# Performance work log

Measured on AMD Instinct MI355X. Metric: run time of the kernel, lower is better.

The kernel has to match this reference:

```python
import jax, jax.numpy as jnp
import numpy as np

BN_EPS = 1e-5


def setup_inputs() -> dict:
    key = jax.random.key(0)
    ks = jax.random.split(key, 6)
    b, c_out, c_high = 8, 256, 512
    h1 = w1 = 64
    h2 = w2 = 32
    return {
        "fms_low": jax.random.normal(ks[0], (b, c_out, h1, w1), jnp.float32),
        "fms_high": jax.random.normal(ks[1], (b, c_high, h2, w2), jnp.float32),
        "w_conv": jax.random.normal(ks[2], (c_out, c_high), jnp.float32) * (1.0 / np.sqrt(c_high)),
        "bn_gamma": jnp.ones((c_out,), jnp.float32),
        "bn_beta": jnp.zeros((c_out,), jnp.float32),
        "bn_mean": jnp.zeros((c_out,), jnp.float32),
        "bn_var": jnp.ones((c_out,), jnp.float32),
        "fc1_w": jax.random.normal(ks[3], (c_out // 4, c_out), jnp.float32) * (1.0 / np.sqrt(c_out)),
        "fc1_b": jnp.zeros((c_out // 4,), jnp.float32),
        "fc2_w": jax.random.normal(ks[4], (c_out // 4, c_out), jnp.float32) * (1.0 / np.sqrt(c_out)),
        "fc2_b": jnp.zeros((c_out // 4,), jnp.float32),
        "scale": jax.random.normal(ks[5], (1,), jnp.float32),
    }


def reference(fms_low, fms_high, w_conv, bn_gamma, bn_beta, bn_mean, bn_var,
              fc1_w, fc1_b, fc2_w, fc2_b, scale):
    b, c, h1, w1 = fms_low.shape
    # conv_high: 1x1 conv (no bias) + BN (inference) + ReLU
    x = jnp.einsum('bchw,oc->bohw', fms_high, w_conv)  # [b, 256, h2, w2]
    inv = bn_gamma / jnp.sqrt(bn_var + BN_EPS)
    x = x * inv[None, :, None, None] + (bn_beta - bn_mean * inv)[None, :, None, None]
    x = jax.nn.relu(x)
    # raw row-major reshapes, matching torch .view(b, -1, C)
    feat_low = fms_low.reshape(b, -1, c)    # [b, N_low, 256]
    feat_high = x.reshape(b, -1, c)         # [b, N_high, 256]
    mid_low = feat_low @ fc1_w.T + fc1_b    # [b, N_low, 64]
    mid_high = feat_high @ fc2_w.T + fc2_b  # [b, N_high, 64]
    energy = jnp.einsum('bnd,bmd->bnm', mid_low, mid_high)  # [b, N_low, N_high]
    attn = jax.nn.softmax(energy, axis=-1)
    # bmm(feat_high^T, attn^T) -> [b, 256, N_low]
    mid = jnp.einsum('bmc,bnm->bcn', feat_high, attn).reshape(b, c, h1, w1)
    return scale[0] * mid
```

## Files before the change

kernel.cpp:

```cpp
#include <hip/hip_runtime.h>
#include <hip/hip_bf16.h>

typedef __bf16 v8bf __attribute__((ext_vector_type(8)));
typedef float  v4f  __attribute__((ext_vector_type(4)));

typedef __attribute__((address_space(3))) void       lds_vd;
typedef __attribute__((address_space(1))) const void gbl_vd;

#define MFMA16(a, b, c) __builtin_amdgcn_mfma_f32_16x16x32_bf16(a, b, c, 0, 0, 0)

__device__ __forceinline__ void split_hl(float v, __bf16* h, __bf16* l) {
    __bf16 hh = (__bf16)v;
    *h = hh;
    *l = (__bf16)(v - (float)hh);
}

__device__ __forceinline__ int swz_idx(int row, int col) {
    return row * 64 + ((((col >> 3) ^ (row & 7))) << 3) + (col & 7);
}
__device__ __forceinline__ const __bf16* frag_ptr(const __bf16* base, int row, int g) {
    return base + row * 64 + ((g ^ (row & 7)) << 3);
}


__global__ __launch_bounds__(256) void k_conv(
    const float* __restrict__ FH, const float* __restrict__ W,
    const float* __restrict__ gamma, const float* __restrict__ beta,
    const float* __restrict__ mean, const float* __restrict__ var,
    __bf16* __restrict__ Xhi, __bf16* __restrict__ Xlo, __bf16* __restrict__ VT)
{
    __shared__ __align__(16) __bf16 Ah[64 * 64];
    __shared__ __align__(16) __bf16 Al[64 * 64];
    __shared__ __align__(16) __bf16 Bh[64 * 64];
    __shared__ __align__(16) __bf16 Bl[64 * 64];
    __shared__ float invl[64], shl[64];

    const int tid = threadIdx.x, lane = tid & 63, w = tid >> 6;
    const int l15 = lane & 15, quad = lane >> 4;
    const int u0 = blockIdx.x * 16, o0 = blockIdx.y * 64, b = blockIdx.z;
    const float* FHb = FH + (size_t)b * 524288;

    if (tid < 64) {
        const int o = o0 + tid;
        const float iv = gamma[o] * rsqrtf(var[o] + 1e-5f);
        invl[tid] = iv;
        shl[tid] = beta[o] - mean[o] * iv;
    }

    const int ao = tid >> 2, aseg = tid & 3;
    float wreg[16], freg[16];
    {
        const float* wp = W + (size_t)(o0 + ao) * 512 + aseg * 16;
        #pragma unroll
        for (int q = 0; q < 4; ++q) {
            float4 f = ((const float4*)wp)[q];
            wreg[4*q] = f.x; wreg[4*q+1] = f.y; wreg[4*q+2] = f.z; wreg[4*q+3] = f.w;
        }
        const float* fp = FHb + (size_t)lane * 1024 + w * 256 + u0;
        #pragma unroll
        for (int q = 0; q < 4; ++q) {
            float4 f = ((const float4*)fp)[q];
            freg[4*q] = f.x; freg[4*q+1] = f.y; freg[4*q+2] = f.z; freg[4*q+3] = f.w;
        }
    }

    v4f acc[2][2];
    #pragma unroll
    for (int i = 0; i < 2; ++i)
        #pragma unroll
        for (int j = 0; j < 2; ++j) { v4f z = {0.f,0.f,0.f,0.f}; acc[i][j] = z; }
    const int oh = w >> 1, nh = w & 1;

    for (int ch = 0; ch < 8; ++ch) {
        if (ch) __syncthreads();
        #pragma unroll
        for (int z = 0; z < 2; ++z) {
            v8bf hv, lv;
            #pragma unroll
            for (int e = 0; e < 8; ++e) {
                __bf16 h, l; split_hl(wreg[8*z + e], &h, &l);
                hv[e] = h; lv[e] = l;
            }
            const int gi = (2*aseg + z) ^ (ao & 7);
            *(v8bf*)(Ah + ao*64 + (gi << 3)) = hv;
            *(v8bf*)(Al + ao*64 + (gi << 3)) = lv;
        }
        #pragma unroll
        for (int ul = 0; ul < 16; ++ul) {
            __bf16 h, l; split_hl(freg[ul], &h, &l);
            const int idx = (w*16 + ul)*64 + (((lane >> 3) ^ (ul & 7)) << 3) + (lane & 7);
            Bh[idx] = h; Bl[idx] = l;
        }
        __syncthreads();
        if (ch < 7) {
            const int c1 = (ch + 1) * 64;
            const float* wp = W + (size_t)(o0 + ao) * 512 + c1 + aseg * 16;
            #pragma unroll
            for (int q = 0; q < 4; ++q) {
                float4 f = ((const float4*)wp)[q];
                wreg[4*q] = f.x; wreg[4*q+1] = f.y; wreg[4*q+2] = f.z; wreg[4*q+3] = f.w;
            }
            const float* fp = FHb + (size_t)(c1 + lane) * 1024 + w * 256 + u0;
            #pragma unroll
            for (int q = 0; q < 4; ++q) {
                float4 f = ((const float4*)fp)[q];
                freg[4*q] = f.x; freg[4*q+1] = f.y; freg[4*q+2] = f.z; freg[4*q+3] = f.w;
            }
        }
        #pragma unroll
        for (int ks = 0; ks < 2; ++ks) {
            const int g = 4*ks + quad;
            v8bf a_h[2], a_l[2], b_h[2], b_l[2];
            #pragma unroll
            for (int i = 0; i < 2; ++i) {
                const int row = oh*32 + i*16 + l15;
                a_h[i] = *(const v8bf*)frag_ptr(Ah, row, g);
                a_l[i] = *(const v8bf*)frag_ptr(Al, row, g);
            }
            #pragma unroll
            for (int j = 0; j < 2; ++j) {
                const int row = nh*32 + j*16 + l15;
                b_h[j] = *(const v8bf*)frag_ptr(Bh, row, g);
                b_l[j] = *(const v8bf*)frag_ptr(Bl, row, g);
            }
            #pragma unroll
            for (int i = 0; i < 2; ++i)
                #pragma unroll
                for (int j = 0; j < 2; ++j) {
                    acc[i][j] = MFMA16(a_h[i], b_h[j], acc[i][j]);
                    acc[i][j] = MFMA16(a_h[i], b_l[j], acc[i][j]);
                    acc[i][j] = MFMA16(a_l[i], b_h[j], acc[i][j]);
                }
        }
    }
    __syncthreads();

    #pragma unroll
    for (int i = 0; i < 2; ++i)
        #pragma unroll
        for (int j = 0; j < 2; ++j)
            #pragma unroll
            for (int r = 0; r < 4; ++r) {
                const int row = oh*32 + i*16 + quad*4 + r;
                const int col = nh*32 + j*16 + l15;
                float v = acc[i][j][r] * invl[row] + shl[row];
                v = fmaxf(v, 0.f);
                __bf16 h, l; split_hl(v, &h, &l);
                const int idx = swz_idx(row, col);
                Ah[idx] = h; Al[idx] = l;
            }
    __syncthreads();
    {
        const int o = tid >> 2, pv = tid & 3;
        const size_t gbase = ((size_t)b*256 + o0 + o) * 1024 + pv*256 + u0;
        #pragma unroll
        for (int z = 0; z < 2; ++z) {
            const int gi = (2*pv + z) ^ (o & 7);
            v8bf h = *(v8bf*)(Ah + o*64 + (gi << 3));
            v8bf l = *(v8bf*)(Al + o*64 + (gi << 3));
            *(v8bf*)(Xhi + gbase + z*8) = h;
            *(v8bf*)(Xlo + gbase + z*8) = l;
        }
    }
    {
        const int ul = tid >> 4, s = tid & 15;
        __bf16 tmp[16];
        #pragma unroll
        for (int k = 0; k < 16; ++k) {
            const int m = s*16 + k;
            const int row = m >> 2;
            const int col = (m & 3)*16 + ul;
            tmp[k] = Ah[swz_idx(row, col)];
        }
        __bf16* vp = VT + ((size_t)b*256 + u0 + ul) * 1024 + 4*o0 + s*16;
        *(v8bf*)(vp)     = *(v8bf*)(tmp);
        *(v8bf*)(vp + 8) = *(v8bf*)(tmp + 8);
    }
}

__global__ __launch_bounds__(256) void k_proj32(
    const float* __restrict__ Feat, const float* __restrict__ Wfc,
    const float* __restrict__ bfc,
    __bf16* __restrict__ Ohi, __bf16* __restrict__ Olo)
{
    __shared__ __align__(16) __bf16 Ah[128 * 64], Al[128 * 64];
    __shared__ __align__(16) __bf16 Bh[64 * 64],  Bl[64 * 64];
    const int tid = threadIdx.x, lane = tid & 63, w = tid >> 6;
    const int l15 = lane & 15, quad = lane >> 4;
    const int r0 = blockIdx.x * 128;
    const int arow = tid >> 1, ahalf = tid & 1;
    const int brow = tid >> 2, bseg = tid & 3;

    float areg[32], breg[16];
    {
        const float* ap = Feat + (size_t)(r0 + arow) * 256 + ahalf * 32;
        #pragma unroll
        for (int q = 0; q < 8; ++q) {
            float4 f = ((const float4*)ap)[q];
            areg[4*q] = f.x; areg[4*q+1] = f.y; areg[4*q+2] = f.z; areg[4*q+3] = f.w;
        }
        const float* bp = Wfc + (size_t)brow * 256 + bseg * 16;
        #pragma unroll
        for (int q = 0; q < 4; ++q) {
            float4 f = ((const float4*)bp)[q];
            breg[4*q] = f.x; breg[4*q+1] = f.y; breg[4*q+2] = f.z; breg[4*q+3] = f.w;
        }
    }
    v4f acc[2][4];
    #pragma unroll
    for (int i = 0; i < 2; ++i)
        #pragma unroll
        for (int j = 0; j < 4; ++j) { v4f z = {0.f,0.f,0.f,0.f}; acc[i][j] = z; }

    for (int ch = 0; ch < 4; ++ch) {
        if (ch) __syncthreads();
        #pragma unroll
        for (int z = 0; z < 4; ++z) {
            v8bf hv, lv;
            #pragma unroll
            for (int e = 0; e < 8; ++e) {
                __bf16 h, l; split_hl(areg[8*z + e], &h, &l);
                hv[e] = h; lv[e] = l;
            }
            const int gi = (4*ahalf + z) ^ (arow & 7);
            *(v8bf*)(Ah + arow*64 + (gi << 3)) = hv;
            *(v8bf*)(Al + arow*64 + (gi << 3)) = lv;
        }
        #pragma unroll
        for (int z = 0; z < 2; ++z) {
            v8bf hv, lv;
            #pragma unroll
            for (int e = 0; e < 8; ++e) {
                __bf16 h, l; split_hl(breg[8*z + e], &h, &l);
                hv[e] = h; lv[e] = l;
            }
            const int gi = (2*bseg + z) ^ (brow & 7);
            *(v8bf*)(Bh + brow*64 + (gi << 3)) = hv;
            *(v8bf*)(Bl + brow*64 + (gi << 3)) = lv;
        }
        __syncthreads();
        if (ch < 3) {
            const int c1 = (ch + 1) * 64;
            const float* ap = Feat + (size_t)(r0 + arow) * 256 + c1 + ahalf * 32;
            #pragma unroll
            for (int q = 0; q < 8; ++q) {
                float4 f = ((const float4*)ap)[q];
                areg[4*q] = f.x; areg[4*q+1] = f.y; areg[4*q+2] = f.z; areg[4*q+3] = f.w;
            }
            const float* bp = Wfc + (size_t)brow * 256 + c1 + bseg * 16;
            #pragma unroll
            for (int q = 0; q < 4; ++q) {
                float4 f = ((const float4*)bp)[q];
                breg[4*q] = f.x; breg[4*q+1] = f.y; breg[4*q+2] = f.z; breg[4*q+3] = f.w;
            }
        }
        #pragma unroll
        for (int ks = 0; ks < 2; ++ks) {
            const int g = 4*ks + quad;
            v8bf a_h[2], a_l[2], b_h[4], b_l[4];
            #pragma unroll
            for (int i = 0; i < 2; ++i) {
                const int row = w*32 + i*16 + l15;
                a_h[i] = *(const v8bf*)frag_ptr(Ah, row, g);
                a_l[i] = *(const v8bf*)frag_ptr(Al, row, g);
            }
            #pragma unroll
            for (int j = 0; j < 4; ++j) {
                const int row = j*16 + l15;
                b_h[j] = *(const v8bf*)frag_ptr(Bh, row, g);
                b_l[j] = *(const v8bf*)frag_ptr(Bl, row, g);
            }
            #pragma unroll
            for (int i = 0; i < 2; ++i)
                #pragma unroll
                for (int j = 0; j < 4; ++j) {
                    acc[i][j] = MFMA16(a_h[i], b_h[j], acc[i][j]);
                    acc[i][j] = MFMA16(a_h[i], b_l[j], acc[i][j]);
                    acc[i][j] = MFMA16(a_l[i], b_h[j], acc[i][j]);
                }
        }
    }
    __syncthreads();
    #pragma unroll
    for (int j = 0; j < 4; ++j) {
        const float bias = bfc[j*16 + l15];
        #pragma unroll
        for (int i = 0; i < 2; ++i)
            #pragma unroll
            for (int r = 0; r < 4; ++r) {
                const int row = w*32 + i*16 + quad*4 + r;
                const int col = j*16 + l15;
                __bf16 h, l; split_hl(acc[i][j][r] + bias, &h, &l);
                const int idx = swz_idx(row, col);
                Ah[idx] = h; Al[idx] = l;
            }
    }
    __syncthreads();
    {
        const int row = tid >> 1, half = tid & 1;
        __bf16* oh_ = Ohi + (size_t)(r0 + row) * 64 + half * 32;
        __bf16* ol_ = Olo + (size_t)(r0 + row) * 64 + half * 32;
        #pragma unroll
        for (int z = 0; z < 4; ++z) {
            const int gi = (4*half + z) ^ (row & 7);
            *(v8bf*)(oh_ + z*8) = *(v8bf*)(Ah + row*64 + (gi << 3));
            *(v8bf*)(ol_ + z*8) = *(v8bf*)(Al + row*64 + (gi << 3));
        }
    }
}

__global__ __launch_bounds__(256) void k_projbf(
    const __bf16* __restrict__ Fhi, const __bf16* __restrict__ Flo,
    const float* __restrict__ Wfc, const float* __restrict__ bfc,
    __bf16* __restrict__ Ohi, __bf16* __restrict__ Olo)
{
    __shared__ __align__(16) __bf16 Ah[32 * 64], Al[32 * 64];
    __shared__ __align__(16) __bf16 Bh[64 * 64], Bl[64 * 64];
    const int tid = threadIdx.x, lane = tid & 63, w = tid >> 6;
    const int l15 = lane & 15, quad = lane >> 4;
    const int r0 = blockIdx.x * 32;
    const int srow = tid >> 3, sg = tid & 7;
    const int brow = tid >> 2, bseg = tid & 3;

    float breg[16];
    v8bf ha, la;
    {
        ha = *(const v8bf*)(Fhi + (size_t)(r0 + srow) * 256 + sg * 8);
        la = *(const v8bf*)(Flo + (size_t)(r0 + srow) * 256 + sg * 8);
        const float* bp = Wfc + (size_t)brow * 256 + bseg * 16;
        #pragma unroll
        for (int q = 0; q < 4; ++q) {
            float4 f = ((const float4*)bp)[q];
            breg[4*q] = f.x; breg[4*q+1] = f.y; breg[4*q+2] = f.z; breg[4*q+3] = f.w;
        }
    }
    v4f acc[2];
    { v4f z = {0.f,0.f,0.f,0.f}; acc[0] = z; acc[1] = z; }
    const int mt = w >> 1, nh = w & 1;

    for (int ch = 0; ch < 4; ++ch) {
        if (ch) __syncthreads();
        {
            const int gi = sg ^ (srow & 7);
            *(v8bf*)(Ah + srow*64 + (gi << 3)) = ha;
            *(v8bf*)(Al + srow*64 + (gi << 3)) = la;
        }
        #pragma unroll
        for (int z = 0; z < 2; ++z) {
            v8bf hv, lv;
            #pragma unroll
            for (int e = 0; e < 8; ++e) {
                __bf16 h, l; split_hl(breg[8*z + e], &h, &l);
                hv[e] = h; lv[e] = l;
            }
            const int gi = (2*bseg + z) ^ (brow & 7);
            *(v8bf*)(Bh + brow*64 + (gi << 3)) = hv;
            *(v8bf*)(Bl + brow*64 + (gi << 3)) = lv;
        }
        __syncthreads();
        if (ch < 3) {
            const int c1 = (ch + 1) * 64;
            ha = *(const v8bf*)(Fhi + (size_t)(r0 + srow) * 256 + c1 + sg * 8);
            la = *(const v8bf*)(Flo + (size_t)(r0 + srow) * 256 + c1 + sg * 8);
            const float* bp = Wfc + (size_t)brow * 256 + c1 + bseg * 16;
            #pragma unroll
            for (int q = 0; q < 4; ++q) {
                float4 f = ((const float4*)bp)[q];
                breg[4*q] = f.x; breg[4*q+1] = f.y; breg[4*q+2] = f.z; breg[4*q+3] = f.w;
            }
        }
        #pragma unroll
        for (int ks = 0; ks < 2; ++ks) {
            const int g = 4*ks + quad;
            const int arow = mt*16 + l15;
            v8bf a_h = *(const v8bf*)frag_ptr(Ah, arow, g);
            v8bf a_l = *(const v8bf*)frag_ptr(Al, arow, g);
            #pragma unroll
            for (int j = 0; j < 2; ++j) {
                const int row = (nh*2 + j)*16 + l15;
                v8bf b_h = *(const v8bf*)frag_ptr(Bh, row, g);
                v8bf b_l = *(const v8bf*)frag_ptr(Bl, row, g);
                acc[j] = MFMA16(a_h, b_h, acc[j]);
                acc[j] = MFMA16(a_h, b_l, acc[j]);
                acc[j] = MFMA16(a_l, b_h, acc[j]);
            }
        }
    }
    __syncthreads();
    #pragma unroll
    for (int j = 0; j < 2; ++j) {
        const float bias = bfc[(nh*2 + j)*16 + l15];
        #pragma unroll
        for (int r = 0; r < 4; ++r) {
            const int row = mt*16 + quad*4 + r;
            const int col = (nh*2 + j)*16 + l15;
            __bf16 h, l; split_hl(acc[j][r] + bias, &h, &l);
            const int idx = swz_idx(row, col);
            Ah[idx] = h; Al[idx] = l;
        }
    }
    __syncthreads();
    {
        const int row = tid >> 3, g = tid & 7;
        const int gi = g ^ (row & 7);
        *(v8bf*)(Ohi + (size_t)(r0 + row) * 64 + g*8) = *(v8bf*)(Ah + row*64 + (gi << 3));
        *(v8bf*)(Olo + (size_t)(r0 + row) * 64 + g*8) = *(v8bf*)(Al + row*64 + (gi << 3));
    }
}

__global__ __launch_bounds__(256, 4) void k_attn(
    const __bf16* __restrict__ MLhi, const __bf16* __restrict__ MLlo,
    const __bf16* __restrict__ MHhi, const __bf16* __restrict__ MHlo,
    const __bf16* __restrict__ VT,
    const float* __restrict__ scale_p,
    float* __restrict__ out)
{
    __shared__ __align__(16) __bf16 Khi[32 * 64];
    __shared__ __align__(16) __bf16 Klo[32 * 64];
    __shared__ __align__(16) __bf16 Vs[256 * 32];
    __shared__ __align__(16) __bf16 Ps[4][16 * 32];
    __shared__ float lsh[4][16];

    const int tid = threadIdx.x, lane = tid & 63, w = tid >> 6;
    const int l15 = lane & 15, quad = lane >> 4;
    const int b = blockIdx.x & 7, qtb = blockIdx.x >> 3;
    const int q0 = qtb * 64;

    v8bf qhi[2], qlo[2];
    {
        const __bf16* qp  = MLhi + ((size_t)(b*4096 + q0 + w*16 + l15)) * 64;
        const __bf16* qlp = MLlo + ((size_t)(b*4096 + q0 + w*16 + l15)) * 64;
        #pragma unroll
        for (int h = 0; h < 2; ++h) {
            qhi[h] = *(const v8bf*)(qp + h*32 + quad*8);
            qlo[h] = *(const v8bf*)(qlp + h*32 + quad*8);
        }
    }

    const char* Khg = (const char*)(MHhi + (size_t)b * 65536);
    const char* Klg = (const char*)(MHlo + (size_t)b * 65536);
    const char* Vg  = (const char*)(VT + (size_t)b * 262144);
    const int offK = (lane >> 3) * 128 + (((lane & 7) ^ ((lane >> 3) & 7)) << 4);
    const int offV = (lane >> 2) * 2048 + ((((lane & 3) ^ ((lane >> 3) & 3))) << 4);

    v4f oacc[4][4];
    #pragma unroll
    for (int qt = 0; qt < 4; ++qt)
        #pragma unroll
        for (int cb = 0; cb < 4; ++cb) { v4f z = {0.f,0.f,0.f,0.f}; oacc[qt][cb] = z; }
    float lrow[4] = {0.f, 0.f, 0.f, 0.f};

    for (int ch = 0; ch < 32; ++ch) {
        const int m0 = ch * 32;
        if (ch) __syncthreads();
        if (w < 4) {
            __builtin_amdgcn_global_load_lds((gbl_vd*)(Khg + m0*128 + w*1024 + offK),
                                             (lds_vd*)((char*)Khi + w*1024), 16, 0, 0);
            __builtin_amdgcn_global_load_lds((gbl_vd*)(Klg + m0*128 + w*1024 + offK),
                                             (lds_vd*)((char*)Klo + w*1024), 16, 0, 0);
        }
        #pragma unroll
        for (int i = w; i < 16; i += 4)
            __builtin_amdgcn_global_load_lds((gbl_vd*)(Vg + m0*2 + i*32768 + offV),
                                             (lds_vd*)((char*)Vs + i*1024), 16, 0, 0);
        __syncthreads();

        float S[2][4];
        #pragma unroll
        for (int mb = 0; mb < 2; ++mb) {
            v4f sacc = {0.f, 0.f, 0.f, 0.f};
            #pragma unroll
            for (int h = 0; h < 2; ++h) {
                const int row = mb*16 + l15, g = 4*h + quad;
                v8bf kh = *(const v8bf*)frag_ptr(Khi, row, g);
                v8bf kl = *(const v8bf*)frag_ptr(Klo, row, g);
                sacc = MFMA16(qhi[h], kh, sacc);
                sacc = MFMA16(qhi[h], kl, sacc);
                sacc = MFMA16(qlo[h], kh, sacc);
            }
            #pragma unroll
            for (int r = 0; r < 4; ++r) S[mb][r] = sacc[r];
        }

        #pragma unroll
        for (int mb = 0; mb < 2; ++mb)
            #pragma unroll
            for (int r = 0; r < 4; ++r) {
                const float p = __expf(S[mb][r]);
                S[mb][r] = p;
                lrow[r] += p;
            }
        #pragma unroll
        for (int mb = 0; mb < 2; ++mb)
            #pragma unroll
            for (int r = 0; r < 4; ++r) {
                const int row = quad*4 + r;
                const int slot = (mb*2 + (l15 >> 3)) ^ ((row >> 1) & 3);
                Ps[w][row*32 + (slot << 3) + (l15 & 7)] = (__bf16)S[mb][r];
            }
        __syncthreads();

        v8bf pa[4];
        #pragma unroll
        for (int qt = 0; qt < 4; ++qt)
            pa[qt] = *(const v8bf*)(Ps[qt] + l15*32 + ((quad ^ ((l15 >> 1) & 3)) << 3));
        #pragma unroll
        for (int cb = 0; cb < 4; ++cb) {
            const int vrow = w*64 + cb*16 + l15;
            v8bf vv = *(const v8bf*)(Vs + vrow*32 + ((quad ^ ((vrow >> 1) & 3)) << 3));
            #pragma unroll
            for (int qt = 0; qt < 4; ++qt)
                oacc[qt][cb] = MFMA16(pa[qt], vv, oacc[qt][cb]);
        }
    }

    #pragma unroll
    for (int r = 0; r < 4; ++r) {
        float s = lrow[r];
        #pragma unroll
        for (int d = 1; d < 16; d <<= 1) s += __shfl_xor(s, d, 64);
        lrow[r] = s;
    }
    if (l15 == 0) {
        #pragma unroll
        for (int r = 0; r < 4; ++r) lsh[w][quad*4 + r] = lrow[r];
    }
    __syncthreads();

    const float scl = scale_p[0];
    float inv[4][4];
    #pragma unroll
    for (int qt = 0; qt < 4; ++qt)
        #pragma unroll
        for (int r = 0; r < 4; ++r) inv[qt][r] = scl / lsh[qt][quad*4 + r];
    float* outb = out + (size_t)b * 256 * 4096;
    #pragma unroll
    for (int cb = 0; cb < 4; ++cb) {
        const int c = w*64 + cb*16 + l15;
        #pragma unroll
        for (int qt = 0; qt < 4; ++qt) {
            float4 v;
            v.x = oacc[qt][cb][0] * inv[qt][0];
            v.y = oacc[qt][cb][1] * inv[qt][1];
            v.z = oacc[qt][cb][2] * inv[qt][2];
            v.w = oacc[qt][cb][3] * inv[qt][3];
            *(float4*)(outb + (size_t)c * 4096 + q0 + qt*16 + quad*4) = v;
        }
    }
}

extern "C" void kernel_launch(void* const* d_in, const int* in_sizes, int n_in,
                              void* d_out, int out_size, void* d_ws, size_t ws_size,
                              hipStream_t stream)
{
    const float* fms_low  = (const float*)d_in[0];
    const float* fms_high = (const float*)d_in[1];
    const float* w_conv   = (const float*)d_in[2];
    const float* gamma    = (const float*)d_in[3];
    const float* beta     = (const float*)d_in[4];
    const float* mean     = (const float*)d_in[5];
    const float* var      = (const float*)d_in[6];
    const float* fc1_w    = (const float*)d_in[7];
    const float* fc1_b    = (const float*)d_in[8];
    const float* fc2_w    = (const float*)d_in[9];
    const float* fc2_b    = (const float*)d_in[10];
    const float* scale    = (const float*)d_in[11];
    float* out = (float*)d_out;

    __bf16* Xhi  = (__bf16*)d_ws;
    __bf16* Xlo  = Xhi  + (size_t)8*256*1024;
    __bf16* VT   = Xlo  + (size_t)8*256*1024;
    __bf16* MLhi = VT   + (size_t)8*256*1024;
    __bf16* MLlo = MLhi + (size_t)8*4096*64;
    __bf16* MHhi = MLlo + (size_t)8*4096*64;
    __bf16* MHlo = MHhi + (size_t)8*1024*64;

    k_conv<<<dim3(16, 4, 8), 256, 0, stream>>>(fms_high, w_conv, gamma, beta,
                                               mean, var, Xhi, Xlo, VT);
    k_projbf<<<dim3(256), 256, 0, stream>>>(Xhi, Xlo, fc2_w, fc2_b, MHhi, MHlo);
    k_proj32<<<dim3(256), 256, 0, stream>>>(fms_low, fc1_w, fc1_b, MLhi, MLlo);
    k_attn<<<dim3(512), 256, 0, stream>>>(MLhi, MLlo, MHhi, MHlo, VT, scale, out);
}
```

Measured before the change: 195.7 us.

## Double-buffer conv and attention tiles, restructure projections and attention P layout

The conv kernel now double-buffers its LDS tiles, which drops one barrier per chunk. Both projection kernels now hold the whole split weight in LDS and stream A fragments straight from global memory with no chunk loop. The attention kernel prefetches the next K/V chunk into a second LDS buffer, computes S transposed, and moves P through lane shuffles instead of shared memory. It also makes each wave own 16 queries across all 256 channels, which removes the cross-wave row-sum reduction. The cost is more LDS per block, lower occupancy, and output stores that are scalar and strided.

```diff
diff --git a/kernel.cpp b/kernel.cpp
--- a/kernel.cpp
+++ b/kernel.cpp
@@ -29,10 +29,10 @@
     const float* __restrict__ mean, const float* __restrict__ var,
     __bf16* __restrict__ Xhi, __bf16* __restrict__ Xlo, __bf16* __restrict__ VT)
 {
-    __shared__ __align__(16) __bf16 Ah[64 * 64];
-    __shared__ __align__(16) __bf16 Al[64 * 64];
-    __shared__ __align__(16) __bf16 Bh[64 * 64];
-    __shared__ __align__(16) __bf16 Bl[64 * 64];
+    __shared__ __align__(16) __bf16 Ah[2][64 * 64];
+    __shared__ __align__(16) __bf16 Al[2][64 * 64];
+    __shared__ __align__(16) __bf16 Bh[2][64 * 64];
+    __shared__ __align__(16) __bf16 Bl[2][64 * 64];
     __shared__ float invl[64], shl[64];
 
     const int tid = threadIdx.x, lane = tid & 63, w = tid >> 6;
@@ -72,7 +72,7 @@
     const int oh = w >> 1, nh = w & 1;
 
     for (int ch = 0; ch < 8; ++ch) {
-        if (ch) __syncthreads();
+        const int bf = ch & 1;
         #pragma unroll
         for (int z = 0; z < 2; ++z) {
             v8bf hv, lv;
@@ -82,14 +82,14 @@
                 hv[e] = h; lv[e] = l;
             }
             const int gi = (2*aseg + z) ^ (ao & 7);
-            *(v8bf*)(Ah + ao*64 + (gi << 3)) = hv;
-            *(v8bf*)(Al + ao*64 + (gi << 3)) = lv;
+            *(v8bf*)(Ah[bf] + ao*64 + (gi << 3)) = hv;
+            *(v8bf*)(Al[bf] + ao*64 + (gi << 3)) = lv;
         }
         #pragma unroll
         for (int ul = 0; ul < 16; ++ul) {
             __bf16 h, l; split_hl(freg[ul], &h, &l);
             const int idx = (w*16 + ul)*64 + (((lane >> 3) ^ (ul & 7)) << 3) + (lane & 7);
-            Bh[idx] = h; Bl[idx] = l;
+            Bh[bf][idx] = h; Bl[bf][idx] = l;
         }
         __syncthreads();
         if (ch < 7) {
@@ -114,14 +114,14 @@
             #pragma unroll
             for (int i = 0; i < 2; ++i) {
                 const int row = oh*32 + i*16 + l15;
-                a_h[i] = *(const v8bf*)frag_ptr(Ah, row, g);
-                a_l[i] = *(const v8bf*)frag_ptr(Al, row, g);
+                a_h[i] = *(const v8bf*)frag_ptr(Ah[bf], row, g);
+                a_l[i] = *(const v8bf*)frag_ptr(Al[bf], row, g);
             }
             #pragma unroll
             for (int j = 0; j < 2; ++j) {
                 const int row = nh*32 + j*16 + l15;
-                b_h[j] = *(const v8bf*)frag_ptr(Bh, row, g);
-                b_l[j] = *(const v8bf*)frag_ptr(Bl, row, g);
+                b_h[j] = *(const v8bf*)frag_ptr(Bh[bf], row, g);
+                b_l[j] = *(const v8bf*)frag_ptr(Bl[bf], row, g);
             }
             #pragma unroll
             for (int i = 0; i < 2; ++i)
@@ -147,7 +147,7 @@
                 v = fmaxf(v, 0.f);
                 __bf16 h, l; split_hl(v, &h, &l);
                 const int idx = swz_idx(row, col);
-                Ah[idx] = h; Al[idx] = l;
+                Ah[0][idx] = h; Al[0][idx] = l;
             }
     __syncthreads();
     {
@@ -156,8 +156,8 @@
         #pragma unroll
         for (int z = 0; z < 2; ++z) {
             const int gi = (2*pv + z) ^ (o & 7);
-            v8bf h = *(v8bf*)(Ah + o*64 + (gi << 3));
-            v8bf l = *(v8bf*)(Al + o*64 + (gi << 3));
+            v8bf h = *(v8bf*)(Ah[0] + o*64 + (gi << 3));
+            v8bf l = *(v8bf*)(Al[0] + o*64 + (gi << 3));
             *(v8bf*)(Xhi + gbase + z*8) = h;
             *(v8bf*)(Xlo + gbase + z*8) = l;
         }
@@ -170,7 +170,7 @@
             const int m = s*16 + k;
             const int row = m >> 2;
             const int col = (m & 3)*16 + ul;
-            tmp[k] = Ah[swz_idx(row, col)];
+            tmp[k] = Ah[0][swz_idx(row, col)];
         }
         __bf16* vp = VT + ((size_t)b*256 + u0 + ul) * 1024 + 4*o0 + s*16;
         *(v8bf*)(vp)     = *(v8bf*)(tmp);
@@ -183,128 +183,63 @@
     const float* __restrict__ bfc,
     __bf16* __restrict__ Ohi, __bf16* __restrict__ Olo)
 {
-    __shared__ __align__(16) __bf16 Ah[128 * 64], Al[128 * 64];
-    __shared__ __align__(16) __bf16 Bh[64 * 64],  Bl[64 * 64];
+    __shared__ __align__(16) __bf16 Wh[64 * 256], Wl[64 * 256];
     const int tid = threadIdx.x, lane = tid & 63, w = tid >> 6;
     const int l15 = lane & 15, quad = lane >> 4;
-    const int r0 = blockIdx.x * 128;
-    const int arow = tid >> 1, ahalf = tid & 1;
-    const int brow = tid >> 2, bseg = tid & 3;
-
-    float areg[32], breg[16];
-    {
-        const float* ap = Feat + (size_t)(r0 + arow) * 256 + ahalf * 32;
-        #pragma unroll
-        for (int q = 0; q < 8; ++q) {
-            float4 f = ((const float4*)ap)[q];
-            areg[4*q] = f.x; areg[4*q+1] = f.y; areg[4*q+2] = f.z; areg[4*q+3] = f.w;
-        }
-        const float* bp = Wfc + (size_t)brow * 256 + bseg * 16;
-        #pragma unroll
-        for (int q = 0; q < 4; ++q) {
-            float4 f = ((const float4*)bp)[q];
-            breg[4*q] = f.x; breg[4*q+1] = f.y; breg[4*q+2] = f.z; breg[4*q+3] = f.w;
-        }
-    }
-    v4f acc[2][4];
-    #pragma unroll
-    for (int i = 0; i < 2; ++i)
-        #pragma unroll
-        for (int j = 0; j < 4; ++j) { v4f z = {0.f,0.f,0.f,0.f}; acc[i][j] = z; }
-
-    for (int ch = 0; ch < 4; ++ch) {
-        if (ch) __syncthreads();
-        #pragma unroll
-        for (int z = 0; z < 4; ++z) {
+    const int r0 = blockIdx.x * 64;
+
+    {
+        const int row = tid >> 2, seg = tid & 3;
+        const float* wp = Wfc + (size_t)row * 256 + seg * 64;
+        #pragma unroll
+        for (int z = 0; z < 8; ++z) {
+            float4 f0 = ((const float4*)wp)[2*z];
+            float4 f1 = ((const float4*)wp)[2*z + 1];
+            float e[8] = {f0.x, f0.y, f0.z, f0.w, f1.x, f1.y, f1.z, f1.w};
             v8bf hv, lv;
             #pragma unroll
-            for (int e = 0; e < 8; ++e) {
-                __bf16 h, l; split_hl(areg[8*z + e], &h, &l);
-                hv[e] = h; lv[e] = l;
-            }
-            const int gi = (4*ahalf + z) ^ (arow & 7);
-            *(v8bf*)(Ah + arow*64 + (gi << 3)) = hv;
-            *(v8bf*)(Al + arow*64 + (gi << 3)) = lv;
-        }
-        #pragma unroll
-        for (int z = 0; z < 2; ++z) {
-            v8bf hv, lv;
-            #pragma unroll
-            for (int e = 0; e < 8; ++e) {
-                __bf16 h, l; split_hl(breg[8*z + e], &h, &l);
-                hv[e] = h; lv[e] = l;
-            }
-            const int gi = (2*bseg + z) ^ (brow & 7);
-            *(v8bf*)(Bh + brow*64 + (gi << 3)) = hv;
-            *(v8bf*)(Bl + brow*64 + (gi << 3)) = lv;
-        }
-        __syncthreads();
-        if (ch < 3) {
-            const int c1 = (ch + 1) * 64;
-            const float* ap = Feat + (size_t)(r0 + arow) * 256 + c1 + ahalf * 32;
-            #pragma unroll
-            for (int q = 0; q < 8; ++q) {
-                float4 f = ((const float4*)ap)[q];
-                areg[4*q] = f.x; areg[4*q+1] = f.y; areg[4*q+2] = f.z; areg[4*q+3] = f.w;
-            }
-            const float* bp = Wfc + (size_t)brow * 256 + c1 + bseg * 16;
-            #pragma unroll
-            for (int q = 0; q < 4; ++q) {
-                float4 f = ((const float4*)bp)[q];
-                breg[4*q] = f.x; breg[4*q+1] = f.y; breg[4*q+2] = f.z; breg[4*q+3] = f.w;
-            }
-        }
-        #pragma unroll
-        for (int ks = 0; ks < 2; ++ks) {
-            const int g = 4*ks + quad;
-            v8bf a_h[2], a_l[2], b_h[4], b_l[4];
-            #pragma unroll
-            for (int i = 0; i < 2; ++i) {
-                const int row = w*32 + i*16 + l15;
-                a_h[i] = *(const v8bf*)frag_ptr(Ah, row, g);
-                a_l[i] = *(const v8bf*)frag_ptr(Al, row, g);
-            }
-            #pragma unroll
-            for (int j = 0; j < 4; ++j) {
-                const int row = j*16 + l15;
-                b_h[j] = *(const v8bf*)frag_ptr(Bh, row, g);
-                b_l[j] = *(const v8bf*)frag_ptr(Bl, row, g);
-            }
-            #pragma unroll
-            for (int i = 0; i < 2; ++i)
-                #pragma unroll
-                for (int j = 0; j < 4; ++j) {
-                    acc[i][j] = MFMA16(a_h[i], b_h[j], acc[i][j]);
-                    acc[i][j] = MFMA16(a_h[i], b_l[j], acc[i][j]);
-                    acc[i][j] = MFMA16(a_l[i], b_h[j], acc[i][j]);
-                }
+            for (int k = 0; k < 8; ++k) { __bf16 h, l; split_hl(e[k], &h, &l); hv[k] = h; lv[k] = l; }
+            const int slot = (seg*8 + z) ^ (row & 7);
+            *(v8bf*)(Wh + row*256 + (slot << 3)) = hv;
+            *(v8bf*)(Wl + row*256 + (slot << 3)) = lv;
         }
     }
     __syncthreads();
+
+    const float* ap = Feat + (size_t)(r0 + w*16 + l15) * 256;
+    v4f acc[4];
+    #pragma unroll
+    for (int j = 0; j < 4; ++j) { v4f z = {0.f,0.f,0.f,0.f}; acc[j] = z; }
+
+    #pragma unroll
+    for (int ks = 0; ks < 8; ++ks) {
+        float4 f0 = *(const float4*)(ap + ks*32 + quad*8);
+        float4 f1 = *(const float4*)(ap + ks*32 + quad*8 + 4);
+        float e[8] = {f0.x, f0.y, f0.z, f0.w, f1.x, f1.y, f1.z, f1.w};
+        v8bf ah, al;
+        #pragma unroll
+        for (int k = 0; k < 8; ++k) { __bf16 h, l; split_hl(e[k], &h, &l); ah[k] = h; al[k] = l; }
+        const int gk = ks*4 + quad;
+        #pragma unroll
+        for (int j = 0; j < 4; ++j) {
+            const int row = j*16 + l15;
+            const int slot = gk ^ (row & 7);
+            v8bf bh = *(const v8bf*)(Wh + row*256 + (slot << 3));
+            v8bf bl = *(const v8bf*)(Wl + row*256 + (slot << 3));
+            acc[j] = MFMA16(ah, bh, acc[j]);
+            acc[j] = MFMA16(ah, bl, acc[j]);
+            acc[j] = MFMA16(al, bh, acc[j]);
+        }
+    }
     #pragma unroll
     for (int j = 0; j < 4; ++j) {
         const float bias = bfc[j*16 + l15];
         #pragma unroll
-        for (int i = 0; i < 2; ++i)
-            #pragma unroll
-            for (int r = 0; r < 4; ++r) {
-                const int row = w*32 + i*16 + quad*4 + r;
-                const int col = j*16 + l15;
-                __bf16 h, l; split_hl(acc[i][j][r] + bias, &h, &l);
-                const int idx = swz_idx(row, col);
-                Ah[idx] = h; Al[idx] = l;
-            }
-    }
-    __syncthreads();
-    {
-        const int row = tid >> 1, half = tid & 1;
-        __bf16* oh_ = Ohi + (size_t)(r0 + row) * 64 + half * 32;
-        __bf16* ol_ = Olo + (size_t)(r0 + row) * 64 + half * 32;
-        #pragma unroll
-        for (int z = 0; z < 4; ++z) {
-            const int gi = (4*half + z) ^ (row & 7);
-            *(v8bf*)(oh_ + z*8) = *(v8bf*)(Ah + row*64 + (gi << 3));
-            *(v8bf*)(ol_ + z*8) = *(v8bf*)(Al + row*64 + (gi << 3));
+        for (int r = 0; r < 4; ++r) {
+            const int orow = r0 + w*16 + quad*4 + r;
+            __bf16 h, l; split_hl(acc[j][r] + bias, &h, &l);
+            Ohi[(size_t)orow*64 + j*16 + l15] = h;
+            Olo[(size_t)orow*64 + j*16 + l15] = l;
         }
     }
 }
@@ -314,112 +249,74 @@
     const float* __restrict__ Wfc, const float* __restrict__ bfc,
     __bf16* __restrict__ Ohi, __bf16* __restrict__ Olo)
 {
-    __shared__ __align__(16) __bf16 Ah[32 * 64], Al[32 * 64];
-    __shared__ __align__(16) __bf16 Bh[64 * 64], Bl[64 * 64];
+    __shared__ __align__(16) __bf16 Wh[64 * 256], Wl[64 * 256];
     const int tid = threadIdx.x, lane = tid & 63, w = tid >> 6;
     const int l15 = lane & 15, quad = lane >> 4;
-    const int r0 = blockIdx.x * 32;
-    const int srow = tid >> 3, sg = tid & 7;
-    const int brow = tid >> 2, bseg = tid & 3;
-
-    float breg[16];
-    v8bf ha, la;
-    {
-        ha = *(const v8bf*)(Fhi + (size_t)(r0 + srow) * 256 + sg * 8);
-        la = *(const v8bf*)(Flo + (size_t)(r0 + srow) * 256 + sg * 8);
-        const float* bp = Wfc + (size_t)brow * 256 + bseg * 16;
-        #pragma unroll
-        for (int q = 0; q < 4; ++q) {
-            float4 f = ((const float4*)bp)[q];
-            breg[4*q] = f.x; breg[4*q+1] = f.y; breg[4*q+2] = f.z; breg[4*q+3] = f.w;
-        }
-    }
-    v4f acc[2];
-    { v4f z = {0.f,0.f,0.f,0.f}; acc[0] = z; acc[1] = z; }
-    const int mt = w >> 1, nh = w & 1;
-
-    for (int ch = 0; ch < 4; ++ch) {
-        if (ch) __syncthreads();
-        {
-            const int gi = sg ^ (srow & 7);
-            *(v8bf*)(Ah + srow*64 + (gi << 3)) = ha;
-            *(v8bf*)(Al + srow*64 + (gi << 3)) = la;
-        }
-        #pragma unroll
-        for (int z = 0; z < 2; ++z) {
+    const int r0 = blockIdx.x * 64;
+
+    {
+        const int row = tid >> 2, seg = tid & 3;
+        const float* wp = Wfc + (size_t)row * 256 + seg * 64;
+        #pragma unroll
+        for (int z = 0; z < 8; ++z) {
+            float4 f0 = ((const float4*)wp)[2*z];
+            float4 f1 = ((const float4*)wp)[2*z + 1];
+            float e[8] = {f0.x, f0.y, f0.z, f0.w, f1.x, f1.y, f1.z, f1.w};
             v8bf hv, lv;
             #pragma unroll
-            for (int e = 0; e < 8; ++e) {
-                __bf16 h, l; split_hl(breg[8*z + e], &h, &l);
-                hv[e] = h; lv[e] = l;
-            }
-            const int gi = (2*bseg + z) ^ (brow & 7);
-            *(v8bf*)(Bh + brow*64 + (gi << 3)) = hv;
-            *(v8bf*)(Bl + brow*64 + (gi << 3)) = lv;
-        }
-        __syncthreads();
-        if (ch < 3) {
-            const int c1 = (ch + 1) * 64;
-            ha = *(const v8bf*)(Fhi + (size_t)(r0 + srow) * 256 + c1 + sg * 8);
-            la = *(const v8bf*)(Flo + (size_t)(r0 + srow) * 256 + c1 + sg * 8);
-            const float* bp = Wfc + (size_t)brow * 256 + c1 + bseg * 16;
-            #pragma unroll
-            for (int q = 0; q < 4; ++q) {
-                float4 f = ((const float4*)bp)[q];
-                breg[4*q] = f.x; breg[4*q+1] = f.y; breg[4*q+2] = f.z; breg[4*q+3] = f.w;
-            }
-        }
-        #pragma unroll
-        for (int ks = 0; ks < 2; ++ks) {
-            const int g = 4*ks + quad;
-            const int arow = mt*16 + l15;
-            v8bf a_h = *(const v8bf*)frag_ptr(Ah, arow, g);
-            v8bf a_l = *(const v8bf*)frag_ptr(Al, arow, g);
-            #pragma unroll
-            for (int j = 0; j < 2; ++j) {
-                const int row = (nh*2 + j)*16 + l15;
-                v8bf b_h = *(const v8bf*)frag_ptr(Bh, row, g);
-                v8bf b_l = *(const v8bf*)frag_ptr(Bl, row, g);
-                acc[j] = MFMA16(a_h, b_h, acc[j]);
-                acc[j] = MFMA16(a_h, b_l, acc[j]);
-                acc[j] = MFMA16(a_l, b_h, acc[j]);
-            }
+            for (int k = 0; k < 8; ++k) { __bf16 h, l; split_hl(e[k], &h, &l); hv[k] = h; lv[k] = l; }
+            const int slot = (seg*8 + z) ^ (row & 7);
+            *(v8bf*)(Wh + row*256 + (slot << 3)) = hv;
+            *(v8bf*)(Wl + row*256 + (slot << 3)) = lv;
         }
     }
     __syncthreads();
-    #pragma unroll
-    for (int j = 0; j < 2; ++j) {
-        const float bias = bfc[(nh*2 + j)*16 + l15];
+
+    const __bf16* aph = Fhi + (size_t)(r0 + w*16 + l15) * 256;
+    const __bf16* apl = Flo + (size_t)(r0 + w*16 + l15) * 256;
+    v4f acc[4];
+    #pragma unroll
+    for (int j = 0; j < 4; ++j) { v4f z = {0.f,0.f,0.f,0.f}; acc[j] = z; }
+
+    #pragma unroll
+    for (int ks = 0; ks < 8; ++ks) {
+        v8bf ah = *(const v8bf*)(aph + ks*32 + quad*8);
+        v8bf al = *(const v8bf*)(apl + ks*32 + quad*8);
+        const int gk = ks*4 + quad;
+        #pragma unroll
+        for (int j = 0; j < 4; ++j) {
+            const int row = j*16 + l15;
+            const int slot = gk ^ (row & 7);
+            v8bf bh = *(const v8bf*)(Wh + row*256 + (slot << 3));
+            v8bf bl = *(const v8bf*)(Wl + row*256 + (slot << 3));
+            acc[j] = MFMA16(ah, bh, acc[j]);
+            acc[j] = MFMA16(ah, bl, acc[j]);
+            acc[j] = MFMA16(al, bh, acc[j]);
+        }
+    }
+    #pragma unroll
+    for (int j = 0; j < 4; ++j) {
+        const float bias = bfc[j*16 + l15];
         #pragma unroll
         for (int r = 0; r < 4; ++r) {
-            const int row = mt*16 + quad*4 + r;
-            const int col = (nh*2 + j)*16 + l15;
+            const int orow = r0 + w*16 + quad*4 + r;
             __bf16 h, l; split_hl(acc[j][r] + bias, &h, &l);
-            const int idx = swz_idx(row, col);
-            Ah[idx] = h; Al[idx] = l;
-        }
-    }
-    __syncthreads();
-    {
-        const int row = tid >> 3, g = tid & 7;
-        const int gi = g ^ (row & 7);
-        *(v8bf*)(Ohi + (size_t)(r0 + row) * 64 + g*8) = *(v8bf*)(Ah + row*64 + (gi << 3));
-        *(v8bf*)(Olo + (size_t)(r0 + row) * 64 + g*8) = *(v8bf*)(Al + row*64 + (gi << 3));
-    }
-}
-
-__global__ __launch_bounds__(256, 4) void k_attn(
+            Ohi[(size_t)orow*64 + j*16 + l15] = h;
+            Olo[(size_t)orow*64 + j*16 + l15] = l;
+        }
+    }
+}
+
+__global__ __launch_bounds__(256) void k_attn(
     const __bf16* __restrict__ MLhi, const __bf16* __restrict__ MLlo,
     const __bf16* __restrict__ MHhi, const __bf16* __restrict__ MHlo,
     const __bf16* __restrict__ VT,
     const float* __restrict__ scale_p,
     float* __restrict__ out)
 {
-    __shared__ __align__(16) __bf16 Khi[32 * 64];
-    __shared__ __align__(16) __bf16 Klo[32 * 64];
-    __shared__ __align__(16) __bf16 Vs[256 * 32];
-    __shared__ __align__(16) __bf16 Ps[4][16 * 32];
-    __shared__ float lsh[4][16];
+    __shared__ __align__(16) __bf16 Khi[2][32 * 64];
+    __shared__ __align__(16) __bf16 Klo[2][32 * 64];
+    __shared__ __align__(16) __bf16 Vs[2][256 * 32];
 
     const int tid = threadIdx.x, lane = tid & 63, w = tid >> 6;
     const int l15 = lane & 15, quad = lane >> 4;
@@ -443,108 +340,93 @@
     const int offK = (lane >> 3) * 128 + (((lane & 7) ^ ((lane >> 3) & 7)) << 4);
     const int offV = (lane >> 2) * 2048 + ((((lane & 3) ^ ((lane >> 3) & 3))) << 4);
 
-    v4f oacc[4][4];
-    #pragma unroll
-    for (int qt = 0; qt < 4; ++qt)
-        #pragma unroll
-        for (int cb = 0; cb < 4; ++cb) { v4f z = {0.f,0.f,0.f,0.f}; oacc[qt][cb] = z; }
-    float lrow[4] = {0.f, 0.f, 0.f, 0.f};
+    v4f oacc[16];
+    #pragma unroll
+    for (int ct = 0; ct < 16; ++ct) { v4f z = {0.f,0.f,0.f,0.f}; oacc[ct] = z; }
+    float lrow = 0.f;
+
+    const int srcA = l15 + (((2*quad) & 3) << 4);
+    const int srcB = l15 + (((2*quad + 1) & 3) << 4);
+    const bool hi_mb = ((quad >> 1) & 1) != 0;
+
+    {
+        __builtin_amdgcn_global_load_lds((gbl_vd*)(Khg + w*1024 + offK),
+                                         (lds_vd*)((char*)Khi[0] + w*1024), 16, 0, 0);
+        __builtin_amdgcn_global_load_lds((gbl_vd*)(Klg + w*1024 + offK),
+                                         (lds_vd*)((char*)Klo[0] + w*1024), 16, 0, 0);
+        for (int i = w; i < 16; i += 4)
+            __builtin_amdgcn_global_load_lds((gbl_vd*)(Vg + i*32768 + offV),
+                                             (lds_vd*)((char*)Vs[0] + i*1024), 16, 0, 0);
+    }
 
     for (int ch = 0; ch < 32; ++ch) {
-        const int m0 = ch * 32;
-        if (ch) __syncthreads();
-        if (w < 4) {
+        const int bf = ch & 1;
+        __syncthreads();
+        if (ch < 31) {
+            const int m0 = (ch + 1) * 32, nb = bf ^ 1;
             __builtin_amdgcn_global_load_lds((gbl_vd*)(Khg + m0*128 + w*1024 + offK),
-                                             (lds_vd*)((char*)Khi + w*1024), 16, 0, 0);
+                                             (lds_vd*)((char*)Khi[nb] + w*1024), 16, 0, 0);
             __builtin_amdgcn_global_load_lds((gbl_vd*)(Klg + m0*128 + w*1024 + offK),
-                                             (lds_vd*)((char*)Klo + w*1024), 16, 0, 0);
-        }
-        #pragma unroll
-        for (int i = w; i < 16; i += 4)
-            __builtin_amdgcn_global_load_lds((gbl_vd*)(Vg + m0*2 + i*32768 + offV),
-                                             (lds_vd*)((char*)Vs + i*1024), 16, 0, 0);
-        __syncthreads();
-
-        float S[2][4];
-        #pragma unroll
-        for (int mb = 0; mb < 2; ++mb) {
-            v4f sacc = {0.f, 0.f, 0.f, 0.f};
-            #pragma unroll
-            for (int h = 0; h < 2; ++h) {
-                const int row = mb*16 + l15, g = 4*h + quad;
-                v8bf kh = *(const v8bf*)frag_ptr(Khi, row, g);
-                v8bf kl = *(const v8bf*)frag_ptr(Klo, row, g);
-                sacc = MFMA16(qhi[h], kh, sacc);
-                sacc = MFMA16(qhi[h], kl, sacc);
-                sacc = MFMA16(qlo[h], kh, sacc);
-            }
-            #pragma unroll
-            for (int r = 0; r < 4; ++r) S[mb][r] = sacc[r];
-        }
-
-        #pragma unroll
-        for (int mb = 0; mb < 2; ++mb)
-            #pragma unroll
-            for (int r = 0; r < 4; ++r) {
-                const float p = __expf(S[mb][r]);
-                S[mb][r] = p;
-                lrow[r] += p;
-            }
-        #pragma unroll
-        for (int mb = 0; mb < 2; ++mb)
-            #pragma unroll
-            for (int r = 0; r < 4; ++r) {
-                const int row = quad*4 + r;
-                const int slot = (mb*2 + (l15 >> 3)) ^ ((row >> 1) & 3);
-                Ps[w][row*32 + (slot << 3) + (l15 & 7)] = (__bf16)S[mb][r];
-            }
-        __syncthreads();
-
-        v8bf pa[4];
-        #pragma unroll
-        for (int qt = 0; qt < 4; ++qt)
-            pa[qt] = *(const v8bf*)(Ps[qt] + l15*32 + ((quad ^ ((l15 >> 1) & 3)) << 3));
-        #pragma unroll
-        for (int cb = 0; cb < 4; ++cb) {
-            const int vrow = w*64 + cb*16 + l15;
-            v8bf vv = *(const v8bf*)(Vs + vrow*32 + ((quad ^ ((vrow >> 1) & 3)) << 3));
-            #pragma unroll
-            for (int qt = 0; qt < 4; ++qt)
-                oacc[qt][cb] = MFMA16(pa[qt], vv, oacc[qt][cb]);
-        }
-    }
-
-    #pragma unroll
-    for (int r = 0; r < 4; ++r) {
-        float s = lrow[r];
-        #pragma unroll
-        for (int d = 1; d < 16; d <<= 1) s += __shfl_xor(s, d, 64);
-        lrow[r] = s;
-    }
-    if (l15 == 0) {
-        #pragma unroll
-        for (int r = 0; r < 4; ++r) lsh[w][quad*4 + r] = lrow[r];
-    }
-    __syncthreads();
-
-    const float scl = scale_p[0];
-    float inv[4][4];
-    #pragma unroll
-    for (int qt = 0; qt < 4; ++qt)
-        #pragma unroll
-        for (int r = 0; r < 4; ++r) inv[qt][r] = scl / lsh[qt][quad*4 + r];
-    float* outb = out + (size_t)b * 256 * 4096;
-    #pragma unroll
-    for (int cb = 0; cb < 4; ++cb) {
-        const int c = w*64 + cb*16 + l15;
-        #pragma unroll
-        for (int qt = 0; qt < 4; ++qt) {
-            float4 v;
-            v.x = oacc[qt][cb][0] * inv[qt][0];
-            v.y = oacc[qt][cb][1] * inv[qt][1];
-            v.z = oacc[qt][cb][2] * inv[qt][2];
-            v.w = oacc[qt][cb][3] * inv[qt][3];
-            *(float4*)(outb + (size_t)c * 4096 + q0 + qt*16 + quad*4) = v;
+                                             (lds_vd*)((char*)Klo[nb] + w*1024), 16, 0, 0);
+            for (int i = w; i < 16; i += 4)
+                __builtin_amdgcn_global_load_lds((gbl_vd*)(Vg + m0*2 + i*32768 + offV),
+                                                 (lds_vd*)((char*)Vs[nb] + i*1024), 16, 0, 0);
+        }
+
+        v4f s0 = {0.f,0.f,0.f,0.f}, s1 = {0.f,0.f,0.f,0.f};
+        #pragma unroll
+        for (int h = 0; h < 2; ++h) {
+            const int g = h*4 + quad;
+            v8bf kh0 = *(const v8bf*)frag_ptr(Khi[bf], l15,      g);
+            v8bf kl0 = *(const v8bf*)frag_ptr(Klo[bf], l15,      g);
+            v8bf kh1 = *(const v8bf*)frag_ptr(Khi[bf], 16 + l15, g);
+            v8bf kl1 = *(const v8bf*)frag_ptr(Klo[bf], 16 + l15, g);
+            s0 = MFMA16(kh0, qhi[h], s0);
+            s0 = MFMA16(kl0, qhi[h], s0);
+            s0 = MFMA16(kh0, qlo[h], s0);
+            s1 = MFMA16(kh1, qhi[h], s1);
+            s1 = MFMA16(kl1, qhi[h], s1);
+            s1 = MFMA16(kh1, qlo[h], s1);
+        }
+
+        float P0[4], P1[4];
+        #pragma unroll
+        for (int r = 0; r < 4; ++r) {
+            P0[r] = __expf(s0[r]);
+            P1[r] = __expf(s1[r]);
+            lrow += P0[r] + P1[r];
+        }
+
+        v8bf pf;
+        #pragma unroll
+        for (int r = 0; r < 4; ++r) {
+            const float a0 = __shfl(P0[r], srcA, 64);
+            const float a1 = __shfl(P1[r], srcA, 64);
+            pf[r] = (__bf16)(hi_mb ? a1 : a0);
+            const float b0 = __shfl(P0[r], srcB, 64);
+            const float b1 = __shfl(P1[r], srcB, 64);
+            pf[4 + r] = (__bf16)(hi_mb ? b1 : b0);
+        }
+
+        #pragma unroll
+        for (int ct = 0; ct < 16; ++ct) {
+            const int vrow = ct*16 + l15;
+            v8bf vv = *(const v8bf*)(Vs[bf] + vrow*32 + ((quad ^ ((vrow >> 1) & 3)) << 3));
+            oacc[ct] = MFMA16(vv, pf, oacc[ct]);
+        }
+    }
+
+    lrow += __shfl_xor(lrow, 16, 64);
+    lrow += __shfl_xor(lrow, 32, 64);
+    const float invq = scale_p[0] / lrow;
+
+    float* outb = out + (size_t)b * 256 * 4096 + q0 + w*16 + l15;
+    #pragma unroll
+    for (int ct = 0; ct < 16; ++ct) {
+        #pragma unroll
+        for (int r = 0; r < 4; ++r) {
+            const int c = ct*16 + quad*4 + r;
+            outb[(size_t)c * 4096] = oacc[ct][r] * invq;
         }
     }
 }
@@ -577,7 +459,7 @@
 
     k_conv<<<dim3(16, 4, 8), 256, 0, stream>>>(fms_high, w_conv, gamma, beta,
                                                mean, var, Xhi, Xlo, VT);
-    k_projbf<<<dim3(256), 256, 0, stream>>>(Xhi, Xlo, fc2_w, fc2_b, MHhi, MHlo);
-    k_proj32<<<dim3(256), 256, 0, stream>>>(fms_low, fc1_w, fc1_b, MLhi, MLlo);
+    k_projbf<<<dim3(128), 256, 0, stream>>>(Xhi, Xlo, fc2_w, fc2_b, MHhi, MHlo);
+    k_proj32<<<dim3(512), 256, 0, stream>>>(fms_low, fc1_w, fc1_b, MLhi, MLlo);
     k_attn<<<dim3(512), 256, 0, stream>>>(MLhi, MLlo, MHhi, MHlo, VT, scale, out);
 }
```

Measured after the change: 197.0 us. Within noise of the previous version (+0.7%).
